# Performance work log

Measured on AMD Instinct MI355X. Metric: run time of the kernel, lower is better.

## Reference

```python
import jax, jax.numpy as jnp
import numpy as np

# Conv config matching init_kwargs
C_IN, C_OUT = 128, 256
KH, KW = 3, 3
STRIDE = (1, 1)
PADDING = ((1, 1), (1, 1))
DILATION = (1, 1)
B, H, W = 32, 56, 56


def setup_inputs() -> dict:
    key = jax.random.key(0)
    k1, k2, k3 = jax.random.split(key, 3)
    x = jax.random.normal(k1, (B, C_IN, H, W), dtype=jnp.float32)
    # Flattened weight as stored by Conv2DUF: conv.weight.view(O,-1).t() -> [C*kh*kw, O]
    weight = jax.random.normal(k2, (C_IN * KH * KW, C_OUT), dtype=jnp.float32) * 0.02
    bias = jax.random.normal(k3, (C_OUT,), dtype=jnp.float32) * 0.02
    return {"x": x, "weight": weight, "bias": bias}


def reference(x, weight, bias):
    # Conv2DUF computes unfold(x) @ weight + bias, which is exactly a 2D
    # cross-correlation with the original conv kernel. Recover the [O,C,kh,kw]
    # kernel from the flattened [C*kh*kw, O] matrix and use the fused conv
    # primitive (same math, no giant im2col buffer).
    kernel = weight.T.reshape(C_OUT, C_IN, KH, KW)
    out = jax.lax.conv_general_dilated(
        x, kernel,
        window_strides=STRIDE,
        padding=PADDING,
        rhs_dilation=DILATION,
        dimension_numbers=("NCHW", "OIHW", "NCHW"),
    )
    return out + bias[None, :, None, None]
```

## Files before the change

### kernel.cpp

```cpp
#include <hip/hip_runtime.h>
#include <stdint.h>


#define C_INQ 128
#define C_OUTQ 256
#define HDIM 56
#define WDIM 56
#define BDIM 32
#define HP 58
#define WP 58
#define HWPIX (HDIM * WDIM)
#define GSTRIDE (BDIM * HP * WP * 8)
#define XT_ELEMS ((size_t)16 * GSTRIDE)
#define XT_BYTES (XT_ELEMS * 2)

typedef __bf16 bf16x8 __attribute__((ext_vector_type(8)));
typedef unsigned short ushort8 __attribute__((ext_vector_type(8)));
typedef float floatx4 __attribute__((ext_vector_type(4)));

__device__ __forceinline__ unsigned short f2bf(float f) {
  union { float f; unsigned int u; } v; v.f = f;
  unsigned int u = v.u;
  unsigned int r = u + 0x7FFFu + ((u >> 16) & 1u);
  return (unsigned short)(r >> 16);
}
__device__ __forceinline__ unsigned int pack2(float a, float b) {
  return (unsigned int)f2bf(a) | ((unsigned int)f2bf(b) << 16);
}

#define PAD_BLOCKS (BDIM * HP)
__global__ __launch_bounds__(256) void prep_kernel(
    const float* __restrict__ x, unsigned short* __restrict__ xt,
    const float* __restrict__ w, unsigned short* __restrict__ wt) {
  const int t = threadIdx.x;
  if (blockIdx.x < PAD_BLOCKS) {
    const int blk = blockIdx.x;
    const int b = blk / HP;
    const int hp = blk - b * HP;
    uint4* __restrict__ xt4 = (uint4*)xt;
    if (hp == 0 || hp == HP - 1) {
      for (int i = t; i < 16 * WP; i += 256) {
        int g = i / WP, wp = i - g * WP;
        xt4[((size_t)(g * BDIM + b) * HP + hp) * WP + wp] = make_uint4(0, 0, 0, 0);
      }
      return;
    }
    const int h = hp - 1;
    if (t < 224) {
      const int g = t / 14;
      const int w4 = (t - g * 14) * 4;
      const float* xp = x + ((size_t)b * C_INQ + g * 8) * HWPIX + h * WDIM + w4;
      float4 L0 = *(const float4*)(xp);
      float4 L1 = *(const float4*)(xp + HWPIX);
      float4 L2 = *(const float4*)(xp + 2 * HWPIX);
      float4 L3 = *(const float4*)(xp + 3 * HWPIX);
      float4 L4 = *(const float4*)(xp + 4 * HWPIX);
      float4 L5 = *(const float4*)(xp + 5 * HWPIX);
      float4 L6 = *(const float4*)(xp + 6 * HWPIX);
      float4 L7 = *(const float4*)(xp + 7 * HWPIX);
      uint4* dst = xt4 + ((size_t)(g * BDIM + b) * HP + hp) * WP + 1 + w4;
      dst[0] = make_uint4(pack2(L0.x, L1.x), pack2(L2.x, L3.x),
                          pack2(L4.x, L5.x), pack2(L6.x, L7.x));
      dst[1] = make_uint4(pack2(L0.y, L1.y), pack2(L2.y, L3.y),
                          pack2(L4.y, L5.y), pack2(L6.y, L7.y));
      dst[2] = make_uint4(pack2(L0.z, L1.z), pack2(L2.z, L3.z),
                          pack2(L4.z, L5.z), pack2(L6.z, L7.z));
      dst[3] = make_uint4(pack2(L0.w, L1.w), pack2(L2.w, L3.w),
                          pack2(L4.w, L5.w), pack2(L6.w, L7.w));
    } else {
      const int r = t - 224;
      const int g = r >> 1;
      const int wp = (r & 1) * (WP - 1);
      xt4[((size_t)(g * BDIM + b) * HP + hp) * WP + wp] = make_uint4(0, 0, 0, 0);
    }
  } else {
    const int bx = blockIdx.x - PAD_BLOCKS;
    const int khw = bx >> 4;
    const int r4 = bx & 15;
    const int n0w = (r4 >> 2) * 64;
    const int c32 = (r4 & 3) * 32;
    __shared__ float lds[32 * 66];
#pragma unroll
    for (int r = 0; r < 8; ++r) {
      int idx = r * 256 + t;
      int n = idx & 63, c = idx >> 6;
      lds[c * 66 + n] = w[(size_t)((c32 + c) * 9 + khw) * C_OUTQ + n0w + n];
    }
    __syncthreads();
    {
      int n = t >> 2, c8 = (t & 3) * 8;
      const float* s = lds + c8 * 66 + n;
      uint4 o;
      o.x = pack2(s[0],   s[66]);
      o.y = pack2(s[132], s[198]);
      o.z = pack2(s[264], s[330]);
      o.w = pack2(s[396], s[462]);
      *(uint4*)(wt + (size_t)khw * (C_OUTQ * C_INQ) + (size_t)(n0w + n) * C_INQ + c32 + c8) = o;
    }
  }
}

#define BM 256
#define BN 256
#define BK 64
#define NT 18

__global__ __launch_bounds__(512, 2) void conv_gemm_kernel(
    const unsigned short* __restrict__ xt,
    const unsigned short* __restrict__ wt,
    const float* __restrict__ bias,
    float* __restrict__ out) {
  __shared__ __align__(16) unsigned short ldsA[2 * BM * BK];
  __shared__ __align__(16) unsigned short ldsB[2 * BN * BK];

  const int t = threadIdx.x;
  const int lane = t & 63;
  const int wave = t >> 6;
  const int tile_m = blockIdx.x;

  int gbaseA[4], gbaseB[4];
#pragma unroll
  for (int r = 0; r < 4; ++r) {
    int g = r * 512 + t;
    int row = g >> 3;
    int kpart = (g & 7) ^ (row & 7);
    int pix = tile_m * BM + row;
    int b = pix / HWPIX;
    int p = pix - b * HWPIX;
    int h = p / WDIM;
    int w = p - h * WDIM;
    gbaseA[r] = kpart * GSTRIDE + ((b * HP + h) * WP + w) * 8;
  }
#pragma unroll
  for (int r = 0; r < 4; ++r) {
    int g = r * 512 + t;
    int n = g >> 3;
    int kpart = (g & 7) ^ (n & 7);
    gbaseB[r] = n * C_INQ + kpart * 8;
  }

  const int wm = (wave >> 2) * 128;
  const int wn = (wave & 3) * 64;
  const int mrow = lane & 15;
  const int quad = lane >> 4;
  const int xorv = mrow & 7;
  const int kx0 = (quad ^ xorv) * 8;
  const int kx1 = ((4 + quad) ^ xorv) * 8;

  floatx4 acc[8][4] = {};

  auto stage = [&](int kt, int buf) {
    const int khw = kt >> 1;
    const int chalf = kt & 1;
    const int kh = khw / 3;
    const int kw = khw - kh * 3;
    const int koffA = chalf * 8 * GSTRIDE + (kh * WP + kw) * 8;
    const int koffB = khw * (C_OUTQ * C_INQ) + chalf * 64;
    const int ldst = t * 8;
#pragma unroll
    for (int r = 0; r < 4; ++r)
      __builtin_amdgcn_global_load_lds(
          (const __attribute__((address_space(1))) unsigned int*)(xt + gbaseA[r] + koffA),
          (__attribute__((address_space(3))) unsigned int*)(ldsA + buf * (BM * BK) + r * 4096 + ldst),
          16, 0, 0);
#pragma unroll
    for (int r = 0; r < 4; ++r)
      __builtin_amdgcn_global_load_lds(
          (const __attribute__((address_space(1))) unsigned int*)(wt + gbaseB[r] + koffB),
          (__attribute__((address_space(3))) unsigned int*)(ldsB + buf * (BN * BK) + r * 4096 + ldst),
          16, 0, 0);
  };

  auto compute_tile = [&](int buf) {
    const unsigned short* A = ldsA + buf * (BM * BK);
    const unsigned short* B = ldsB + buf * (BN * BK);
    bf16x8 bfr[4][2];
#pragma unroll
    for (int j = 0; j < 4; ++j) {
      const unsigned short* br = B + (wn + j * 16 + mrow) * BK;
      bfr[j][0] = __builtin_bit_cast(bf16x8, *(const ushort8*)(br + kx0));
      bfr[j][1] = __builtin_bit_cast(bf16x8, *(const ushort8*)(br + kx1));
    }
#pragma unroll
    for (int p = 0; p < 4; ++p) {
      bf16x8 af[2][2];
#pragma unroll
      for (int i2 = 0; i2 < 2; ++i2) {
        const unsigned short* ar = A + (wm + (p * 2 + i2) * 16 + mrow) * BK;
        af[i2][0] = __builtin_bit_cast(bf16x8, *(const ushort8*)(ar + kx0));
        af[i2][1] = __builtin_bit_cast(bf16x8, *(const ushort8*)(ar + kx1));
      }
      __builtin_amdgcn_s_setprio(1);
#pragma unroll
      for (int i2 = 0; i2 < 2; ++i2)
#pragma unroll
        for (int u = 0; u < 2; ++u)
#pragma unroll
          for (int j = 0; j < 4; ++j)
            acc[p * 2 + i2][j] = __builtin_amdgcn_mfma_f32_16x16x32_bf16(
                af[i2][u], bfr[j][u], acc[p * 2 + i2][j], 0, 0, 0);
      __builtin_amdgcn_s_setprio(0);
    }
  };

#define K_STEP(T, BUF, VM, DOSTAGE)                                  \
  {                                                                  \
    asm volatile("s_waitcnt vmcnt(" VM ")" ::: "memory");            \
    __builtin_amdgcn_s_barrier();                                    \
    compute_tile(BUF);                                               \
    __builtin_amdgcn_s_barrier();                                    \
    if (DOSTAGE) stage((T) + 2, BUF);                                \
  }

  stage(0, 0);
  stage(1, 1);

#pragma unroll 1
  for (int tt = 0; tt < 16; tt += 2) {
    K_STEP(tt, 0, "8", true);
    K_STEP(tt + 1, 1, "8", true);
  }
  K_STEP(16, 0, "8", false);
  K_STEP(17, 1, "0", false);
#undef K_STEP

  float bv[4];
#pragma unroll
  for (int j = 0; j < 4; ++j) bv[j] = bias[wn + j * 16 + mrow];
#pragma unroll
  for (int i = 0; i < 8; ++i) {
    const int mbase = tile_m * BM + wm + i * 16 + quad * 4;
    const int b = mbase / HWPIX;
    const int p = mbase - b * HWPIX;
    float* obase = out + (size_t)b * (C_OUTQ * HWPIX) + p;
#pragma unroll
    for (int j = 0; j < 4; ++j) {
      const int ng = wn + j * 16 + mrow;
      floatx4 v = acc[i][j];
      v[0] += bv[j]; v[1] += bv[j]; v[2] += bv[j]; v[3] += bv[j];
      *(floatx4*)(obase + (size_t)ng * HWPIX) = v;
    }
  }
}

extern "C" void kernel_launch(void* const* d_in, const int* in_sizes, int n_in,
                              void* d_out, int out_size, void* d_ws, size_t ws_size,
                              hipStream_t stream) {
  const float* x    = (const float*)d_in[0];
  const float* w    = (const float*)d_in[1];
  const float* bias = (const float*)d_in[2];
  float* out = (float*)d_out;

  unsigned short* xt = (unsigned short*)d_ws;
  unsigned short* wt = (unsigned short*)((char*)d_ws + XT_BYTES);

  hipLaunchKernelGGL(prep_kernel, dim3(PAD_BLOCKS + 144), dim3(256), 0, stream,
                     x, xt, w, wt);
  hipLaunchKernelGGL(conv_gemm_kernel, dim3(392), dim3(512), 0, stream,
                     xt, wt, bias, out);
}
```

Baseline: 232.1 us.

## Restructure GEMM K-loop into quadrant-interleaved MFMA phases with split A/B prefetch

Replaces the two-tile-ahead double-buffered K loop with a one-tile-ahead scheme. Each K tile is split into four MFMA quadrant phases separated by barriers, and the A and B global-to-LDS loads for the next tile are issued separately between the phases. Fragment LDS reads are interleaved with the compute phases to cut register pressure and overlap LDS reads with MFMA work. The cost is more barriers per tile and a shorter prefetch distance, since each tile now waits on vmcnt(0), which may expose global load latency.

Measured after the change: 228.8 us. Within noise of the previous version (-1.5%).

```diff
diff --git a/kernel.cpp b/kernel.cpp
--- a/kernel.cpp
+++ b/kernel.cpp
@@ -104,6 +104,8 @@
 #define BN 256
 #define BK 64
 #define NT 18
+#define LDS_HALF 8192
+#define LDS_BUF  16384
 
 __global__ __launch_bounds__(512, 2) void conv_gemm_kernel(
     const unsigned short* __restrict__ xt,
@@ -118,25 +120,22 @@
   const int wave = t >> 6;
   const int tile_m = blockIdx.x;
 
-  int gbaseA[4], gbaseB[4];
-#pragma unroll
-  for (int r = 0; r < 4; ++r) {
+  int gbaseA[2][2], gbaseB[2][2];
+#pragma unroll
+  for (int r = 0; r < 2; ++r) {
     int g = r * 512 + t;
-    int row = g >> 3;
-    int kpart = (g & 7) ^ (row & 7);
-    int pix = tile_m * BM + row;
-    int b = pix / HWPIX;
-    int p = pix - b * HWPIX;
-    int h = p / WDIM;
-    int w = p - h * WDIM;
-    gbaseA[r] = kpart * GSTRIDE + ((b * HP + h) * WP + w) * 8;
-  }
-#pragma unroll
-  for (int r = 0; r < 4; ++r) {
-    int g = r * 512 + t;
-    int n = g >> 3;
-    int kpart = (g & 7) ^ (n & 7);
-    gbaseB[r] = n * C_INQ + kpart * 8;
+    int rl = g >> 3;
+    int kp = (g & 7) ^ (rl & 7);
+#pragma unroll
+    for (int h = 0; h < 2; ++h) {
+      int pix = tile_m * BM + h * 128 + rl;
+      int b = pix / HWPIX;
+      int p = pix - b * HWPIX;
+      int hh = p / WDIM;
+      int ww = p - hh * WDIM;
+      gbaseA[h][r] = kp * GSTRIDE + ((b * HP + hh) * WP + ww) * 8;
+      gbaseB[h][r] = (h * 128 + rl) * C_INQ + kp * 8;
+    }
   }
 
   const int wm = (wave >> 2) * 128;
@@ -146,83 +145,130 @@
   const int xorv = mrow & 7;
   const int kx0 = (quad ^ xorv) * 8;
   const int kx1 = ((4 + quad) ^ xorv) * 8;
+  int abase[8], bbase[4];
+#pragma unroll
+  for (int i = 0; i < 8; ++i) abase[i] = (wm + i * 16 + mrow) * BK;
+#pragma unroll
+  for (int j = 0; j < 4; ++j) bbase[j] = (wn + j * 16 + mrow) * BK;
 
   floatx4 acc[8][4] = {};
 
-  auto stage = [&](int kt, int buf) {
-    const int khw = kt >> 1;
-    const int chalf = kt & 1;
-    const int kh = khw / 3;
-    const int kw = khw - kh * 3;
-    const int koffA = chalf * 8 * GSTRIDE + (kh * WP + kw) * 8;
-    const int koffB = khw * (C_OUTQ * C_INQ) + chalf * 64;
-    const int ldst = t * 8;
-#pragma unroll
-    for (int r = 0; r < 4; ++r)
-      __builtin_amdgcn_global_load_lds(
-          (const __attribute__((address_space(1))) unsigned int*)(xt + gbaseA[r] + koffA),
-          (__attribute__((address_space(3))) unsigned int*)(ldsA + buf * (BM * BK) + r * 4096 + ldst),
-          16, 0, 0);
-#pragma unroll
-    for (int r = 0; r < 4; ++r)
-      __builtin_amdgcn_global_load_lds(
-          (const __attribute__((address_space(1))) unsigned int*)(wt + gbaseB[r] + koffB),
-          (__attribute__((address_space(3))) unsigned int*)(ldsB + buf * (BN * BK) + r * 4096 + ldst),
-          16, 0, 0);
+  auto stageA = [&](int kt, int buf) {
+    const int khw = kt >> 1, ch = kt & 1;
+    const int kh = khw / 3, kw = khw - kh * 3;
+    const int koff = ch * 8 * GSTRIDE + (kh * WP + kw) * 8;
+    unsigned short* base = ldsA + buf * LDS_BUF;
+#pragma unroll
+    for (int h = 0; h < 2; ++h)
+#pragma unroll
+      for (int r = 0; r < 2; ++r)
+        __builtin_amdgcn_global_load_lds(
+            (const __attribute__((address_space(1))) unsigned int*)(xt + gbaseA[h][r] + koff),
+            (__attribute__((address_space(3))) unsigned int*)(base + h * LDS_HALF + r * 4096 + t * 8),
+            16, 0, 0);
   };
-
-  auto compute_tile = [&](int buf) {
-    const unsigned short* A = ldsA + buf * (BM * BK);
-    const unsigned short* B = ldsB + buf * (BN * BK);
-    bf16x8 bfr[4][2];
-#pragma unroll
-    for (int j = 0; j < 4; ++j) {
-      const unsigned short* br = B + (wn + j * 16 + mrow) * BK;
-      bfr[j][0] = __builtin_bit_cast(bf16x8, *(const ushort8*)(br + kx0));
-      bfr[j][1] = __builtin_bit_cast(bf16x8, *(const ushort8*)(br + kx1));
-    }
-#pragma unroll
-    for (int p = 0; p < 4; ++p) {
-      bf16x8 af[2][2];
-#pragma unroll
-      for (int i2 = 0; i2 < 2; ++i2) {
-        const unsigned short* ar = A + (wm + (p * 2 + i2) * 16 + mrow) * BK;
-        af[i2][0] = __builtin_bit_cast(bf16x8, *(const ushort8*)(ar + kx0));
-        af[i2][1] = __builtin_bit_cast(bf16x8, *(const ushort8*)(ar + kx1));
-      }
-      __builtin_amdgcn_s_setprio(1);
-#pragma unroll
-      for (int i2 = 0; i2 < 2; ++i2)
-#pragma unroll
-        for (int u = 0; u < 2; ++u)
-#pragma unroll
-          for (int j = 0; j < 4; ++j)
-            acc[p * 2 + i2][j] = __builtin_amdgcn_mfma_f32_16x16x32_bf16(
-                af[i2][u], bfr[j][u], acc[p * 2 + i2][j], 0, 0, 0);
-      __builtin_amdgcn_s_setprio(0);
-    }
+  auto stageB = [&](int kt, int buf) {
+    const int khw = kt >> 1, ch = kt & 1;
+    const int koff = khw * (C_OUTQ * C_INQ) + ch * 64;
+    unsigned short* base = ldsB + buf * LDS_BUF;
+#pragma unroll
+    for (int h = 0; h < 2; ++h)
+#pragma unroll
+      for (int r = 0; r < 2; ++r)
+        __builtin_amdgcn_global_load_lds(
+            (const __attribute__((address_space(1))) unsigned int*)(wt + gbaseB[h][r] + koff),
+            (__attribute__((address_space(3))) unsigned int*)(base + h * LDS_HALF + r * 4096 + t * 8),
+            16, 0, 0);
   };
 
-#define K_STEP(T, BUF, VM, DOSTAGE)                                  \
-  {                                                                  \
-    asm volatile("s_waitcnt vmcnt(" VM ")" ::: "memory");            \
-    __builtin_amdgcn_s_barrier();                                    \
-    compute_tile(BUF);                                               \
-    __builtin_amdgcn_s_barrier();                                    \
-    if (DOSTAGE) stage((T) + 2, BUF);                                \
-  }
-
-  stage(0, 0);
-  stage(1, 1);
+#define BC8(p) __builtin_bit_cast(bf16x8, *(const ushort8*)(p))
+#define BARW __builtin_amdgcn_s_barrier()
+
+  auto ktile = [&](int T, int buf, bool dostage) {
+    const unsigned short* Ab = ldsA + buf * LDS_BUF;
+    const unsigned short* Bb = ldsB + buf * LDS_BUF;
+    bf16x8 af[4][2], b0[2][2], b1[2][2];
+#pragma unroll
+    for (int i = 0; i < 4; ++i) {
+      af[i][0] = BC8(Ab + abase[i] + kx0);
+      af[i][1] = BC8(Ab + abase[i] + kx1);
+    }
+#pragma unroll
+    for (int j = 0; j < 2; ++j) {
+      b0[j][0] = BC8(Bb + bbase[j] + kx0);
+      b0[j][1] = BC8(Bb + bbase[j] + kx1);
+    }
+    if (dostage) stageA(T + 1, buf ^ 1);
+    BARW;
+    __builtin_amdgcn_s_setprio(1);
+#pragma unroll
+    for (int u = 0; u < 2; ++u)
+#pragma unroll
+      for (int i = 0; i < 4; ++i)
+#pragma unroll
+        for (int j = 0; j < 2; ++j)
+          acc[i][j] = __builtin_amdgcn_mfma_f32_16x16x32_bf16(af[i][u], b0[j][u], acc[i][j], 0, 0, 0);
+    __builtin_amdgcn_s_setprio(0);
+    BARW;
+#pragma unroll
+    for (int j = 0; j < 2; ++j) {
+      b1[j][0] = BC8(Bb + bbase[2 + j] + kx0);
+      b1[j][1] = BC8(Bb + bbase[2 + j] + kx1);
+    }
+    if (dostage) stageB(T + 1, buf ^ 1);
+    BARW;
+    __builtin_amdgcn_s_setprio(1);
+#pragma unroll
+    for (int u = 0; u < 2; ++u)
+#pragma unroll
+      for (int i = 0; i < 4; ++i)
+#pragma unroll
+        for (int j = 0; j < 2; ++j)
+          acc[i][2 + j] = __builtin_amdgcn_mfma_f32_16x16x32_bf16(af[i][u], b1[j][u], acc[i][2 + j], 0, 0, 0);
+    __builtin_amdgcn_s_setprio(0);
+    BARW;
+#pragma unroll
+    for (int i = 0; i < 4; ++i) {
+      af[i][0] = BC8(Ab + abase[4 + i] + kx0);
+      af[i][1] = BC8(Ab + abase[4 + i] + kx1);
+    }
+    BARW;
+    __builtin_amdgcn_s_setprio(1);
+#pragma unroll
+    for (int u = 0; u < 2; ++u)
+#pragma unroll
+      for (int i = 0; i < 4; ++i)
+#pragma unroll
+        for (int j = 0; j < 2; ++j)
+          acc[4 + i][2 + j] = __builtin_amdgcn_mfma_f32_16x16x32_bf16(af[i][u], b1[j][u], acc[4 + i][2 + j], 0, 0, 0);
+    __builtin_amdgcn_s_setprio(0);
+    BARW;
+#pragma unroll
+    for (int u = 0; u < 2; ++u)
+#pragma unroll
+      for (int i = 0; i < 4; ++i)
+#pragma unroll
+        for (int j = 0; j < 2; ++j)
+          acc[4 + i][j] = __builtin_amdgcn_mfma_f32_16x16x32_bf16(af[i][u], b0[j][u], acc[4 + i][j], 0, 0, 0);
+    if (dostage) asm volatile("s_waitcnt vmcnt(0)" ::: "memory");
+    BARW;
+  };
+
+  stageA(0, 0);
+  stageB(0, 0);
+  asm volatile("s_waitcnt vmcnt(0)" ::: "memory");
+  BARW;
 
 #pragma unroll 1
   for (int tt = 0; tt < 16; tt += 2) {
-    K_STEP(tt, 0, "8", true);
-    K_STEP(tt + 1, 1, "8", true);
+    ktile(tt, 0, true);
+    ktile(tt + 1, 1, true);
   }
-  K_STEP(16, 0, "8", false);
-  K_STEP(17, 1, "0", false);
-#undef K_STEP
+  ktile(16, 0, true);
+  ktile(17, 1, false);
+
+#undef BC8
+#undef BARW
 
   float bv[4];
 #pragma unroll
```

## Load halo input region once per block and reuse across all nine filter taps

Applied to the files above, without the earlier changes.

Each block now covers one image and four output rows (224 pixels, 448 blocks) and loads the padded 6x58 halo for all input channels into LDS once. All 9 kernel positions then read the A fragments from that halo at shifted offsets, so only the weight tiles are streamed and double-buffered per K step. This cuts global/L2 traffic for the activation operand by about 9x. The cost is a larger A LDS footprint, a 7-row M tile per wave instead of 8, and an unswizzled A read pattern that may cause LDS bank conflicts. Block indices are also remapped in an XCD-aware order.

Measured after the change: 212.8 us. 8.3% less time.

```diff
diff --git a/kernel.cpp b/kernel.cpp
--- a/kernel.cpp
+++ b/kernel.cpp
@@ -100,145 +100,146 @@
   }
 }
 
-#define BM 256
-#define BN 256
-#define BK 64
-#define NT 18
+#define REGG 352
+#define AGRAN (16 * REGG)
+#define NTILE 18
 
 __global__ __launch_bounds__(512, 2) void conv_gemm_kernel(
     const unsigned short* __restrict__ xt,
     const unsigned short* __restrict__ wt,
     const float* __restrict__ bias,
     float* __restrict__ out) {
-  __shared__ __align__(16) unsigned short ldsA[2 * BM * BK];
-  __shared__ __align__(16) unsigned short ldsB[2 * BN * BK];
+  __shared__ __align__(16) unsigned short ldsA[AGRAN * 8];
+  __shared__ __align__(16) unsigned short ldsB[2 * 2048 * 8];
 
   const int t = threadIdx.x;
   const int lane = t & 63;
   const int wave = t >> 6;
-  const int tile_m = blockIdx.x;
-
-  int gbaseA[4], gbaseB[4];
+  const int bid = ((int)blockIdx.x & 7) * 56 + ((int)blockIdx.x >> 3);
+  const int b = bid / 14;
+  const int ht = bid - b * 14;
+  const int hp0 = ht * 4;
+
+  int gbaseB[4];
 #pragma unroll
   for (int r = 0; r < 4; ++r) {
     int g = r * 512 + t;
     int row = g >> 3;
-    int kpart = (g & 7) ^ (row & 7);
-    int pix = tile_m * BM + row;
-    int b = pix / HWPIX;
-    int p = pix - b * HWPIX;
-    int h = p / WDIM;
-    int w = p - h * WDIM;
-    gbaseA[r] = kpart * GSTRIDE + ((b * HP + h) * WP + w) * 8;
-  }
-#pragma unroll
-  for (int r = 0; r < 4; ++r) {
-    int g = r * 512 + t;
-    int n = g >> 3;
-    int kpart = (g & 7) ^ (n & 7);
-    gbaseB[r] = n * C_INQ + kpart * 8;
-  }
-
-  const int wm = (wave >> 2) * 128;
+    int kp = (g & 7) ^ (row & 7);
+    gbaseB[r] = row * C_INQ + kp * 8;
+  }
+
+  const int wm = (wave >> 2) * 112;
   const int wn = (wave & 3) * 64;
   const int mrow = lane & 15;
   const int quad = lane >> 4;
-  const int xorv = mrow & 7;
-  const int kx0 = (quad ^ xorv) * 8;
-  const int kx1 = ((4 + quad) ^ xorv) * 8;
-
-  floatx4 acc[8][4] = {};
-
-  auto stage = [&](int kt, int buf) {
-    const int khw = kt >> 1;
-    const int chalf = kt & 1;
-    const int kh = khw / 3;
-    const int kw = khw - kh * 3;
-    const int koffA = chalf * 8 * GSTRIDE + (kh * WP + kw) * 8;
-    const int koffB = khw * (C_OUTQ * C_INQ) + chalf * 64;
-    const int ldst = t * 8;
+  const int kxor = mrow & 7;
+  const int kx0 = (quad ^ kxor) * 8;
+  const int kx1 = ((4 + quad) ^ kxor) * 8;
+
+  int agb[7];
+#pragma unroll
+  for (int i = 0; i < 7; ++i) {
+    int m = wm + i * 16 + mrow;
+    int lh = m / 56;
+    int w = m - lh * 56;
+    agb[i] = quad * REGG + lh * 58 + w;
+  }
+  int bbase[4];
+#pragma unroll
+  for (int j = 0; j < 4; ++j) bbase[j] = (wn + j * 16 + mrow) * 64;
+
+  floatx4 acc[7][4] = {};
+
+#pragma unroll
+  for (int r = 0; r < 11; ++r) {
+    int G = r * 512 + t;
+    int gi = G / REGG;
+    int q = G - gi * REGG;
+    if (q >= 6 * 58) q = 0;
+    const unsigned short* src =
+        xt + ((size_t)(gi * BDIM + b) * (HP * WP) + hp0 * WP + q) * 8;
+    __builtin_amdgcn_global_load_lds(
+        (const __attribute__((address_space(1))) unsigned int*)src,
+        (__attribute__((address_space(3))) unsigned int*)(ldsA + G * 8),
+        16, 0, 0);
+  }
+
+  auto stageB = [&](int kt) {
+    const int khw = kt >> 1, ch = kt & 1;
+    const int koff = khw * (C_OUTQ * C_INQ) + ch * 64;
+    unsigned short* base = ldsB + (kt & 1) * 16384;
 #pragma unroll
     for (int r = 0; r < 4; ++r)
       __builtin_amdgcn_global_load_lds(
-          (const __attribute__((address_space(1))) unsigned int*)(xt + gbaseA[r] + koffA),
-          (__attribute__((address_space(3))) unsigned int*)(ldsA + buf * (BM * BK) + r * 4096 + ldst),
-          16, 0, 0);
-#pragma unroll
-    for (int r = 0; r < 4; ++r)
-      __builtin_amdgcn_global_load_lds(
-          (const __attribute__((address_space(1))) unsigned int*)(wt + gbaseB[r] + koffB),
-          (__attribute__((address_space(3))) unsigned int*)(ldsB + buf * (BN * BK) + r * 4096 + ldst),
+          (const __attribute__((address_space(1))) unsigned int*)(wt + gbaseB[r] + koff),
+          (__attribute__((address_space(3))) unsigned int*)(base + r * 4096 + t * 8),
           16, 0, 0);
   };
 
-  auto compute_tile = [&](int buf) {
-    const unsigned short* A = ldsA + buf * (BM * BK);
-    const unsigned short* B = ldsB + buf * (BN * BK);
+  stageB(0);
+  stageB(1);
+
+#define BC8(p) __builtin_bit_cast(bf16x8, *(const ushort8*)(p))
+
+  auto compute = [&](int kt) {
+    const int khw = kt >> 1, ch = kt & 1;
+    const int kh = khw / 3, kw = khw - kh * 3;
+    const int kadd0 = ch * (8 * REGG) + kh * 58 + kw;
+    const unsigned short* Bb = ldsB + (kt & 1) * 16384;
     bf16x8 bfr[4][2];
 #pragma unroll
     for (int j = 0; j < 4; ++j) {
-      const unsigned short* br = B + (wn + j * 16 + mrow) * BK;
-      bfr[j][0] = __builtin_bit_cast(bf16x8, *(const ushort8*)(br + kx0));
-      bfr[j][1] = __builtin_bit_cast(bf16x8, *(const ushort8*)(br + kx1));
-    }
-#pragma unroll
-    for (int p = 0; p < 4; ++p) {
-      bf16x8 af[2][2];
-#pragma unroll
-      for (int i2 = 0; i2 < 2; ++i2) {
-        const unsigned short* ar = A + (wm + (p * 2 + i2) * 16 + mrow) * BK;
-        af[i2][0] = __builtin_bit_cast(bf16x8, *(const ushort8*)(ar + kx0));
-        af[i2][1] = __builtin_bit_cast(bf16x8, *(const ushort8*)(ar + kx1));
-      }
-      __builtin_amdgcn_s_setprio(1);
-#pragma unroll
-      for (int i2 = 0; i2 < 2; ++i2)
-#pragma unroll
-        for (int u = 0; u < 2; ++u)
-#pragma unroll
-          for (int j = 0; j < 4; ++j)
-            acc[p * 2 + i2][j] = __builtin_amdgcn_mfma_f32_16x16x32_bf16(
-                af[i2][u], bfr[j][u], acc[p * 2 + i2][j], 0, 0, 0);
-      __builtin_amdgcn_s_setprio(0);
-    }
+      bfr[j][0] = BC8(Bb + bbase[j] + kx0);
+      bfr[j][1] = BC8(Bb + bbase[j] + kx1);
+    }
+    __builtin_amdgcn_s_setprio(1);
+#pragma unroll
+    for (int i = 0; i < 7; ++i) {
+      bf16x8 a0 = BC8(ldsA + (agb[i] + kadd0) * 8);
+      bf16x8 a1 = BC8(ldsA + (agb[i] + kadd0 + 4 * REGG) * 8);
+#pragma unroll
+      for (int j = 0; j < 4; ++j)
+        acc[i][j] = __builtin_amdgcn_mfma_f32_16x16x32_bf16(a0, bfr[j][0], acc[i][j], 0, 0, 0);
+#pragma unroll
+      for (int j = 0; j < 4; ++j)
+        acc[i][j] = __builtin_amdgcn_mfma_f32_16x16x32_bf16(a1, bfr[j][1], acc[i][j], 0, 0, 0);
+    }
+    __builtin_amdgcn_s_setprio(0);
   };
 
-#define K_STEP(T, BUF, VM, DOSTAGE)                                  \
+#define K_STEP(KT, VM, DOSTAGE)                                      \
   {                                                                  \
     asm volatile("s_waitcnt vmcnt(" VM ")" ::: "memory");            \
     __builtin_amdgcn_s_barrier();                                    \
-    compute_tile(BUF);                                               \
+    compute(KT);                                                     \
     __builtin_amdgcn_s_barrier();                                    \
-    if (DOSTAGE) stage((T) + 2, BUF);                                \
-  }
-
-  stage(0, 0);
-  stage(1, 1);
+    if (DOSTAGE) stageB((KT) + 2);                                   \
+  }
 
 #pragma unroll 1
   for (int tt = 0; tt < 16; tt += 2) {
-    K_STEP(tt, 0, "8", true);
-    K_STEP(tt + 1, 1, "8", true);
-  }
-  K_STEP(16, 0, "8", false);
-  K_STEP(17, 1, "0", false);
+    K_STEP(tt, "4", true);
+    K_STEP(tt + 1, "4", true);
+  }
+  K_STEP(16, "4", false);
+  K_STEP(17, "0", false);
 #undef K_STEP
+#undef BC8
 
   float bv[4];
 #pragma unroll
   for (int j = 0; j < 4; ++j) bv[j] = bias[wn + j * 16 + mrow];
-#pragma unroll
-  for (int i = 0; i < 8; ++i) {
-    const int mbase = tile_m * BM + wm + i * 16 + quad * 4;
-    const int b = mbase / HWPIX;
-    const int p = mbase - b * HWPIX;
-    float* obase = out + (size_t)b * (C_OUTQ * HWPIX) + p;
+  float* ob = out + (size_t)b * (C_OUTQ * HWPIX) + ht * 224;
+#pragma unroll
+  for (int i = 0; i < 7; ++i) {
+    const int mloc = wm + i * 16 + quad * 4;
 #pragma unroll
     for (int j = 0; j < 4; ++j) {
-      const int ng = wn + j * 16 + mrow;
+      const int n = wn + j * 16 + mrow;
       floatx4 v = acc[i][j];
       v[0] += bv[j]; v[1] += bv[j]; v[2] += bv[j]; v[3] += bv[j];
-      *(floatx4*)(obase + (size_t)ng * HWPIX) = v;
+      *(floatx4*)(ob + (size_t)n * HWPIX + mloc) = v;
     }
   }
 }
@@ -256,6 +257,6 @@
 
   hipLaunchKernelGGL(prep_kernel, dim3(PAD_BLOCKS + 144), dim3(256), 0, stream,
                      x, xt, w, wt);
-  hipLaunchKernelGGL(conv_gemm_kernel, dim3(392), dim3(512), 0, stream,
+  hipLaunchKernelGGL(conv_gemm_kernel, dim3(448), dim3(512), 0, stream,
                      xt, wt, bias, out);
 }
```
